# Kernel optimization log

Hardware: AMD Instinct MI355X
Metric: run time of the kernel (lower is better)

The kernel has to match this reference:

```python
import jax, jax.numpy as jnp
import numpy as np

EMBED_DIM = 1024
NUM_HEADS = 16
HEAD_DIM = EMBED_DIM // NUM_HEADS


def setup_inputs() -> dict:
    key = jax.random.key(0)
    ks = jax.random.split(key, 9)
    s = 1.0 / np.sqrt(EMBED_DIM)
    X = jax.random.normal(ks[0], (4, 2048, EMBED_DIM), dtype=jnp.float32)
    # Linear weights stored as [in, out] for x @ W + b
    Wq = jax.random.uniform(ks[1], (EMBED_DIM, EMBED_DIM), jnp.float32, -s, s)
    bq = jax.random.uniform(ks[2], (EMBED_DIM,), jnp.float32, -s, s)
    Wk = jax.random.uniform(ks[3], (EMBED_DIM, EMBED_DIM), jnp.float32, -s, s)
    bk = jax.random.uniform(ks[4], (EMBED_DIM,), jnp.float32, -s, s)
    Wv = jax.random.uniform(ks[5], (EMBED_DIM, EMBED_DIM), jnp.float32, -s, s)
    bv = jax.random.uniform(ks[6], (EMBED_DIM,), jnp.float32, -s, s)
    Wo = jax.random.uniform(ks[7], (EMBED_DIM, EMBED_DIM), jnp.float32, -s, s)
    bo = jax.random.uniform(ks[8], (EMBED_DIM,), jnp.float32, -s, s)
    return {"X": X, "Wq": Wq, "bq": bq, "Wk": Wk, "bk": bk,
            "Wv": Wv, "bv": bv, "Wo": Wo, "bo": bo}


def reference(X, Wq, bq, Wk, bk, Wv, bv, Wo, bo):
    B, S, _ = X.shape
    def split_heads(t):  # [B,S,E] -> [B,H,S,D]
        return t.reshape(B, S, NUM_HEADS, HEAD_DIM).transpose(0, 2, 1, 3)
    Q = split_heads(X @ Wq + bq)
    K = split_heads(X @ Wk + bk)
    V = split_heads(X @ Wv + bv)
    scale = 1.0 / np.sqrt(HEAD_DIM).astype(np.float32)
    scores = jnp.einsum('bhqd,bhkd->bhqk', Q, K) * scale
    probs = jax.nn.softmax(scores, axis=-1)
    attn = jnp.einsum('bhqk,bhkd->bhqd', probs, V)  # [B,H,S,D]
    combined = attn.transpose(0, 2, 1, 3).reshape(B, S, EMBED_DIM)
    return combined @ Wo + bo
```

## Files before the change

kernel.cpp:

```cpp
#include <hip/hip_runtime.h>
#include <hip/hip_bf16.h>

#define EMBED 1024
#define NHEADS 16
#define HDIM 64
#define SEQ 2048
#define BATCH 4
#define ROWS (BATCH * SEQ)

typedef __attribute__((ext_vector_type(8))) short bf16x8;
typedef __attribute__((ext_vector_type(4))) float f32x4;
typedef __attribute__((ext_vector_type(2))) float f32x2;
typedef __attribute__((ext_vector_type(16))) float f32x16;
typedef __attribute__((ext_vector_type(4))) unsigned int u32x4;
typedef __attribute__((ext_vector_type(2))) unsigned int u32x2;
typedef __attribute__((ext_vector_type(2))) int i32x2;
typedef unsigned int u32;

#define SL2E 0.18033688011112042f

__device__ __forceinline__ short f2bf(float f) {
    u32 u = __builtin_bit_cast(u32, f) + 0x8000u;
    return (short)(u >> 16);
}

__device__ __forceinline__ u32 pkbf(float a, float b) {
    u32 ua = __builtin_bit_cast(u32, a) + 0x8000u;
    u32 ub = __builtin_bit_cast(u32, b) + 0x8000u;
    return __builtin_amdgcn_perm(ua, ub, 0x03020706u);
}

__device__ __forceinline__ float fexp2(float x) {
#if __has_builtin(__builtin_amdgcn_exp2f)
    return __builtin_amdgcn_exp2f(x);
#else
    return exp2f(x);
#endif
}

__device__ __forceinline__ void async16(const void* g, void* l) {
    __builtin_amdgcn_global_load_lds((const __attribute__((address_space(1))) u32*)g,
                                     (__attribute__((address_space(3))) u32*)l, 16, 0, 0);
}

__global__ __launch_bounds__(256) void convert_f32_bf16(const float* __restrict__ in,
                                                        short* __restrict__ out) {
    int i = (blockIdx.x * 256 + threadIdx.x) * 4;
    float4 v = *(const float4*)&in[i];
    u32x2 o = { pkbf(v.x, v.y), pkbf(v.z, v.w) };
    *(u32x2*)&out[i] = o;
}

__global__ __launch_bounds__(256) void transpose_w4(const float* __restrict__ W0,
                                                    const float* __restrict__ W1,
                                                    const float* __restrict__ W2,
                                                    const float* __restrict__ W3,
                                                    short* __restrict__ T0,
                                                    short* __restrict__ T1,
                                                    short* __restrict__ T2,
                                                    short* __restrict__ T3) {
    const int z = blockIdx.z;
    const float* W = (z == 0) ? W0 : (z == 1) ? W1 : (z == 2) ? W2 : W3;
    short* WT = (z == 0) ? T0 : (z == 1) ? T1 : (z == 2) ? T2 : T3;
    const float sc = (z == 0) ? SL2E : 1.0f;
    __shared__ float T[64][65];
    const int k0 = blockIdx.y * 64, n0 = blockIdx.x * 64;
    const int rr = threadIdx.x >> 4, cc = (threadIdx.x & 15) * 4;
    #pragma unroll
    for (int p = 0; p < 4; ++p) {
        int r = p * 16 + rr;
        float4 v = *(const float4*)&W[(size_t)(k0 + r) * EMBED + n0 + cc];
        T[r][cc] = v.x * sc; T[r][cc + 1] = v.y * sc; T[r][cc + 2] = v.z * sc; T[r][cc + 3] = v.w * sc;
    }
    __syncthreads();
    #pragma unroll
    for (int p = 0; p < 4; ++p) {
        int r = p * 16 + rr;
        u32x2 o = { pkbf(T[cc][r], T[cc + 1][r]), pkbf(T[cc + 2][r], T[cc + 3][r]) };
        *(u32x2*)&WT[(size_t)(n0 + r) * EMBED + k0 + cc] = o;
    }
}

__global__ __launch_bounds__(512, 2) void gemm256(const short* __restrict__ A,
                                                  const short* __restrict__ BT,
                                                  const float* __restrict__ b0,
                                                  const float* __restrict__ b1,
                                                  const float* __restrict__ b2,
                                                  void* __restrict__ C0,
                                                  void* __restrict__ C1,
                                                  void* __restrict__ C2,
                                                  int mode) {
    __shared__ short As[2][16384];
    __shared__ short Bs[2][16384];
    const int tid = threadIdx.x;
    const int wid = tid >> 6, lane = tid & 63;
    const int c16 = lane & 15, quad = lane >> 4, sw = c16 & 7;
    const int wm = wid >> 2, wn = wid & 3;
    const int rowblk = blockIdx.y * 256, colblk = blockIdx.x * 256;

    const int r0 = tid >> 3;
    const int g0 = (tid & 7) ^ (r0 & 7);
    const short* aS0 = A + (size_t)(rowblk + r0) * EMBED + g0 * 8;
    const short* bS0 = BT + (size_t)(colblk + r0) * EMBED + g0 * 8;

#define STAGE_A(SBUF, H, V) do { \
    const short* _s = aS0 + (size_t)(H) * 131072 + (V) * 64; \
    async16(_s,         &As[SBUF][(H) * 8192 + wid * 512]); \
    async16(_s + 65536, &As[SBUF][(H) * 8192 + wid * 512 + 4096]); \
} while (0)
#define STAGE_B(SBUF, H, V) do { \
    const short* _s = bS0 + (size_t)(H) * 131072 + (V) * 64; \
    async16(_s,         &Bs[SBUF][(H) * 8192 + wid * 512]); \
    async16(_s + 65536, &Bs[SBUF][(H) * 8192 + wid * 512 + 4096]); \
} while (0)

    f32x4 acc[8][4] = {};
    bf16x8 aU[4][2], bE[2][2], bO[2][2];

#define LDA(BUF, MH) do { \
    _Pragma("unroll") \
    for (int fm = 0; fm < 4; ++fm) { \
        const int row = (MH) * 128 + wm * 64 + fm * 16 + c16; \
        _Pragma("unroll") \
        for (int ks = 0; ks < 2; ++ks) \
            aU[fm][ks] = *(const bf16x8*)&As[BUF][row * 64 + ((ks * 4 + quad) ^ sw) * 8]; \
    } \
} while (0)
#define LDB(BUF, NH, DST) do { \
    _Pragma("unroll") \
    for (int fn = 0; fn < 2; ++fn) { \
        const int rowb = (NH) * 128 + wn * 32 + fn * 16 + c16; \
        _Pragma("unroll") \
        for (int ks = 0; ks < 2; ++ks) \
            DST[fn][ks] = *(const bf16x8*)&Bs[BUF][rowb * 64 + ((ks * 4 + quad) ^ sw) * 8]; \
    } \
} while (0)
#define MM(MB, NB, BM_) do { \
    _Pragma("unroll") \
    for (int fm = 0; fm < 4; ++fm) \
        _Pragma("unroll") \
        for (int fn = 0; fn < 2; ++fn) \
            _Pragma("unroll") \
            for (int ks = 0; ks < 2; ++ks) \
                acc[(MB) + fm][(NB) + fn] = \
                    __builtin_amdgcn_mfma_f32_16x16x32_bf16(aU[fm][ks], BM_[fn][ks], \
                        acc[(MB) + fm][(NB) + fn], 0, 0, 0); \
} while (0)
#define PH_MID() do { \
    __builtin_amdgcn_s_barrier(); \
    asm volatile("s_waitcnt lgkmcnt(0)" ::: "memory"); \
    __builtin_amdgcn_s_setprio(1); \
} while (0)
#define PH_END(VM) do { \
    __builtin_amdgcn_s_setprio(0); \
    if (VM) asm volatile("s_waitcnt vmcnt(6)" ::: "memory"); \
    __builtin_amdgcn_s_barrier(); \
} while (0)

    STAGE_B(0, 0, 0); STAGE_A(0, 0, 0); STAGE_A(0, 1, 0); STAGE_B(0, 1, 0);
    STAGE_B(1, 0, 1); STAGE_A(1, 0, 1); STAGE_A(1, 1, 1);
    asm volatile("s_waitcnt vmcnt(6)" ::: "memory");
    __builtin_amdgcn_s_barrier();

    #pragma unroll 1
    for (int it = 0; it < 8; ++it) {
        const int u = 2 * it;
        const int v1 = u + 1, v2 = (u + 2) & 15, v3 = (u + 3) & 15;
        LDA(0, 0); LDB(0, 0, bE); STAGE_B(1, 1, v1); PH_MID(); MM(0, 0, bE); PH_END(0);
        LDB(0, 1, bO);            STAGE_B(0, 0, v2); PH_MID(); MM(0, 2, bO); PH_END(0);
        LDA(0, 1);                STAGE_A(0, 0, v2); PH_MID(); MM(4, 2, bO); PH_END(0);
                 STAGE_A(0, 1, v2); PH_MID(); MM(4, 0, bE); PH_END(1);
        LDA(1, 0); LDB(1, 0, bE); STAGE_B(0, 1, v2); PH_MID(); MM(0, 0, bE); PH_END(0);
        LDB(1, 1, bO);            STAGE_B(1, 0, v3); PH_MID(); MM(0, 2, bO); PH_END(0);
        LDA(1, 1);                STAGE_A(1, 0, v3); PH_MID(); MM(4, 2, bO); PH_END(0);
                 STAGE_A(1, 1, v3); PH_MID(); MM(4, 0, bE); PH_END(1);
    }

    asm volatile("s_waitcnt vmcnt(0)" ::: "memory");

    const int rb0 = rowblk + wm * 64 + quad * 4;
    const int cb0 = wn * 32 + c16;
    if (mode == 0) {
        const int z = colblk >> 10;
        const int cm = colblk & 1023;
        const float* bias = (z == 0) ? b0 : (z == 1) ? b1 : b2;
        if (z == 2) {
            short* Vt = (short*)C2;
            #pragma unroll
            for (int m = 0; m < 8; ++m) {
                const int row = rb0 + (m >> 2) * 128 + (m & 3) * 16;
                const int b = row >> 11, s = row & 2047;
                #pragma unroll
                for (int n = 0; n < 4; ++n) {
                    const int cv = cm + cb0 + (n >> 1) * 128 + (n & 1) * 16;
                    const int head = cv >> 6, d = cv & 63;
                    const float bv = bias[cv];
                    u32x2 o = { pkbf(acc[m][n][0] + bv, acc[m][n][1] + bv),
                                pkbf(acc[m][n][2] + bv, acc[m][n][3] + bv) };
                    *(u32x2*)&Vt[((size_t)(b * NHEADS + head) * HDIM + d) * SEQ + s] = o;
                }
            }
        } else {
            short* Cq = (short*)((z == 0) ? C0 : C1);
            const float bsc = (z == 0) ? SL2E : 1.0f;
            #pragma unroll
            for (int m = 0; m < 8; ++m) {
                const int row = rb0 + (m >> 2) * 128 + (m & 3) * 16;
                #pragma unroll
                for (int n = 0; n < 4; ++n) {
                    const int col = cm + cb0 + (n >> 1) * 128 + (n & 1) * 16;
                    const float bv = bias[col] * bsc;
                    #pragma unroll
                    for (int r = 0; r < 4; ++r)
                        Cq[(size_t)(row + r) * EMBED + col] = f2bf(acc[m][n][r] + bv);
                }
            }
        }
    } else {
        float* Co = (float*)C0;
        #pragma unroll
        for (int m = 0; m < 8; ++m) {
            const int row = rb0 + (m >> 2) * 128 + (m & 3) * 16;
            #pragma unroll
            for (int n = 0; n < 4; ++n) {
                const int col = colblk + cb0 + (n >> 1) * 128 + (n & 1) * 16;
                const float bv = b0[col];
                #pragma unroll
                for (int r = 0; r < 4; ++r)
                    Co[(size_t)(row + r) * EMBED + col] = acc[m][n][r] + bv;
            }
        }
    }
#undef PH_END
#undef PH_MID
#undef MM
#undef LDB
#undef LDA
#undef STAGE_A
#undef STAGE_B
}

__global__ __launch_bounds__(256, 5) void gemm_bf16_128(const short* __restrict__ A,
                                                        const short* __restrict__ BT0,
                                                        const short* __restrict__ BT1,
                                                        const short* __restrict__ BT2,
                                                        const float* __restrict__ b0,
                                                        const float* __restrict__ b1,
                                                        const float* __restrict__ b2,
                                                        void* __restrict__ C0,
                                                        void* __restrict__ C1,
                                                        void* __restrict__ C2,
                                                        int mode) {
    const int z = blockIdx.z;
    const short* BT = (z == 0) ? BT0 : (z == 1) ? BT1 : BT2;
    const float* bias = (z == 0) ? b0 : (z == 1) ? b1 : b2;
    const float bsc = (mode == 0 && z == 0) ? SL2E : 1.0f;
    __shared__ short As[128 * 64];
    __shared__ short Bs[64 * 64];
    const int tid = threadIdx.x;
    const int wave = tid >> 6, lane = tid & 63;
    const int c = lane & 15, quad = lane >> 4;
    const int sw = c & 7;
    const int row0 = blockIdx.y * 128, col0 = blockIdx.x * 64;
    f32x4 acc[2][4] = {};
    for (int k0 = 0; k0 < EMBED; k0 += 64) {
        #pragma unroll
        for (int it = 0; it < 4; ++it) {
            int ci = (it * 4 + wave) * 64 + lane;
            int row = ci >> 3, g = (ci & 7) ^ (row & 7);
            async16(&A[(size_t)(row0 + row) * EMBED + k0 + g * 8], &As[(it * 4 + wave) * 512]);
        }
        #pragma unroll
        for (int it = 0; it < 2; ++it) {
            int ci = (it * 4 + wave) * 64 + lane;
            int row = ci >> 3, g = (ci & 7) ^ (row & 7);
            async16(&BT[(size_t)(col0 + row) * EMBED + k0 + g * 8], &Bs[(it * 4 + wave) * 512]);
        }
        __syncthreads();
        #pragma unroll
        for (int ks = 0; ks < 2; ++ks) {
            bf16x8 af[2], bfr[4];
            #pragma unroll
            for (int i = 0; i < 2; ++i)
                af[i] = *(const bf16x8*)&As[(wave * 32 + i * 16 + c) * 64 + ((ks * 4 + quad) ^ sw) * 8];
            #pragma unroll
            for (int j = 0; j < 4; ++j)
                bfr[j] = *(const bf16x8*)&Bs[(j * 16 + c) * 64 + ((ks * 4 + quad) ^ sw) * 8];
            #pragma unroll
            for (int i = 0; i < 2; ++i)
                #pragma unroll
                for (int j = 0; j < 4; ++j)
                    acc[i][j] = __builtin_amdgcn_mfma_f32_16x16x32_bf16(af[i], bfr[j], acc[i][j], 0, 0, 0);
        }
        __syncthreads();
    }
    if (mode == 0 && z == 2) {
        short* Vt = (short*)C2;
        const int b = row0 >> 11, s0 = (row0 & 2047) + wave * 32;
        const int bh = b * NHEADS + blockIdx.x;
        #pragma unroll
        for (int i = 0; i < 2; ++i)
            #pragma unroll
            for (int j = 0; j < 4; ++j) {
                int d = j * 16 + c;
                float bv = bias[col0 + d];
                int s = s0 + i * 16 + quad * 4;
                u32x2 o = { pkbf(acc[i][j][0] + bv, acc[i][j][1] + bv),
                            pkbf(acc[i][j][2] + bv, acc[i][j][3] + bv) };
                *(u32x2*)&Vt[((size_t)bh * HDIM + d) * SEQ + s] = o;
            }
    } else {
        void* Cout = (z == 0) ? C0 : (z == 1) ? C1 : C2;
        #pragma unroll
        for (int i = 0; i < 2; ++i)
            #pragma unroll
            for (int j = 0; j < 4; ++j) {
                int colb = col0 + j * 16 + c;
                float bv = bias[colb] * bsc;
                #pragma unroll
                for (int r = 0; r < 4; ++r) {
                    int row = row0 + wave * 32 + i * 16 + quad * 4 + r;
                    float v = acc[i][j][r] + bv;
                    if (mode == 0) ((short*)Cout)[(size_t)row * EMBED + colb] = f2bf(v);
                    else           ((float*)Cout)[(size_t)row * EMBED + colb] = v;
                }
            }
    }
}

__global__ __launch_bounds__(256, 3) void attn_mfma(const short* __restrict__ Qb,
                                                    const short* __restrict__ Kb,
                                                    const short* __restrict__ Vt,
                                                    short* __restrict__ Ob) {
    __shared__ short SH[8192];
    short* Ks = SH;
    short* Vs = SH + 4096;
    const int tid = threadIdx.x;
    const int wave = tid >> 6, lane = tid & 63;
    const int l31 = lane & 31, h = lane >> 5;
    const int swz = l31 & 7;
    const int bh = blockIdx.y;
    const int b = bh >> 4, hd = bh & 15;
    const size_t base = (size_t)b * SEQ * EMBED + (size_t)hd * HDIM;
    const size_t vbase = (size_t)bh * HDIM * SEQ;
    const int q0 = blockIdx.x * 128;

    bf16x8 qf[4];
    #pragma unroll
    for (int ks = 0; ks < 4; ++ks)
        qf[ks] = *(const bf16x8*)&Qb[base + (size_t)(q0 + wave * 32 + l31) * EMBED + ks * 16 + h * 8];

    const short* kp[2];
    const short* vp[2];
    int ldofs[2];
    #pragma unroll
    for (int it = 0; it < 2; ++it) {
        int ci = (it * 4 + wave) * 64 + lane;
        int row = ci >> 3, g = (ci & 7) ^ (row & 7);
        kp[it] = Kb + base + (size_t)row * EMBED + g * 8;
        vp[it] = Vt + vbase + (size_t)row * SEQ + g * 8;
        ldofs[it] = (it * 4 + wave) * 512;
    }

    f32x16 O[2] = {};
    f32x2 ls = {0.0f, 0.0f};

    for (int kt = 0; kt < SEQ / 64; ++kt) {
        #pragma unroll
        for (int it = 0; it < 2; ++it) {
            async16(kp[it], &Ks[ldofs[it]]);
            async16(vp[it], &Vs[ldofs[it]]);
            kp[it] += 64 * EMBED;
            vp[it] += 64;
        }
        __syncthreads();

        f32x16 st[2] = {};
        #pragma unroll
        for (int nt = 0; nt < 2; ++nt)
            #pragma unroll
            for (int ks = 0; ks < 4; ++ks) {
                bf16x8 ak = *(const bf16x8*)&Ks[(nt * 32 + l31) * 64 + ((ks * 2 + h) ^ swz) * 8];
                st[nt] = __builtin_amdgcn_mfma_f32_32x32x16_bf16(ak, qf[ks], st[nt], 0, 0, 0);
            }

        u32 pk[2][8];
        #pragma unroll
        for (int nt = 0; nt < 2; ++nt)
            #pragma unroll
            for (int i = 0; i < 8; ++i) {
                float e0 = fexp2(st[nt][2 * i]), e1 = fexp2(st[nt][2 * i + 1]);
                f32x2 e = { e0, e1 };
                ls += e;
                pk[nt][i] = pkbf(e0, e1);
            }

        #pragma unroll
        for (int ks = 0; ks < 4; ++ks) {
            const int nt = ks >> 1, bs = (ks & 1) * 4;
            u32x4 fr;
#if __has_builtin(__builtin_amdgcn_permlane32_swap)
            i32x2 sA = __builtin_amdgcn_permlane32_swap((int)pk[nt][bs + 0], (int)pk[nt][bs + 2], false, false);
            i32x2 sB = __builtin_amdgcn_permlane32_swap((int)pk[nt][bs + 1], (int)pk[nt][bs + 3], false, false);
            fr.x = (u32)sA.x; fr.y = (u32)sB.x; fr.z = (u32)sA.y; fr.w = (u32)sB.y;
#else
            u32 s0 = h ? pk[nt][bs + 0] : pk[nt][bs + 2];
            u32 s1 = h ? pk[nt][bs + 1] : pk[nt][bs + 3];
            u32 r0 = (u32)__shfl_xor((int)s0, 32);
            u32 r1 = (u32)__shfl_xor((int)s1, 32);
            fr.x = h ? r0 : pk[nt][bs + 0];
            fr.y = h ? r1 : pk[nt][bs + 1];
            fr.z = h ? pk[nt][bs + 2] : r0;
            fr.w = h ? pk[nt][bs + 3] : r1;
#endif
            bf16x8 pf = __builtin_bit_cast(bf16x8, fr);
            #pragma unroll
            for (int mt = 0; mt < 2; ++mt) {
                bf16x8 vf = *(const bf16x8*)&Vs[(mt * 32 + l31) * 64 + ((ks * 2 + h) ^ swz) * 8];
                O[mt] = __builtin_amdgcn_mfma_f32_32x32x16_bf16(vf, pf, O[mt], 0, 0, 0);
            }
        }
        __syncthreads();
    }

    float lsum = ls.x + ls.y;
    lsum += __shfl_xor(lsum, 32);
    float inv = 1.0f / lsum;

    const int wbase = wave * 2048;
    #pragma unroll
    for (int mt = 0; mt < 2; ++mt)
        #pragma unroll
        for (int m = 0; m < 4; ++m) {
            u32x2 wv;
            wv.x = pkbf(O[mt][4 * m + 0] * inv, O[mt][4 * m + 1] * inv);
            wv.y = pkbf(O[mt][4 * m + 2] * inv, O[mt][4 * m + 3] * inv);
            int u = mt * 8 + 2 * m + h;
            int su = u ^ ((l31 & 7) << 1);
            *(u32x2*)&SH[wbase + l31 * 64 + su * 4] = wv;
        }
    __syncthreads();
    #pragma unroll
    for (int p = 0; p < 4; ++p) {
        int ci = p * 256 + tid;
        int wq = ci >> 8, rem = ci & 255;
        int r = rem >> 3, cch = rem & 7;
        int su = (2 * cch) ^ ((r & 7) << 1);
        bf16x8 val = *(const bf16x8*)&SH[wq * 2048 + r * 64 + su * 4];
        *(bf16x8*)&Ob[base + (size_t)(q0 + wq * 32 + r) * EMBED + cch * 8] = val;
    }
}

extern "C" void kernel_launch(void* const* d_in, const int* in_sizes, int n_in,
                              void* d_out, int out_size, void* d_ws, size_t ws_size,
                              hipStream_t stream)
{
    const float* X  = (const float*)d_in[0];
    const float* Wq = (const float*)d_in[1];
    const float* bq = (const float*)d_in[2];
    const float* Wk = (const float*)d_in[3];
    const float* bk = (const float*)d_in[4];
    const float* Wv = (const float*)d_in[5];
    const float* bv = (const float*)d_in[6];
    const float* Wo = (const float*)d_in[7];
    const float* bo = (const float*)d_in[8];
    float* out = (float*)d_out;

    const size_t NE = (size_t)ROWS * EMBED;
    short* Xbf = (short*)d_ws;
    short* Qb  = Xbf + NE;
    short* Kb  = Qb + NE;
    short* Vtb = Kb + NE;
    short* WqT = Vtb + NE;
    short* WkT = WqT + (size_t)EMBED * EMBED;
    short* WvT = WkT + (size_t)EMBED * EMBED;
    short* WoT = WvT + (size_t)EMBED * EMBED;

    convert_f32_bf16<<<(ROWS * EMBED) / 1024, 256, 0, stream>>>(X, Xbf);
    dim3 gw(16, 16, 4);
    transpose_w4<<<gw, 256, 0, stream>>>(Wq, Wk, Wv, Wo, WqT, WkT, WvT, WoT);

    dim3 gq(12, 32, 1);
    gemm256<<<gq, 512, 0, stream>>>(Xbf, WqT, bq, bk, bv, Qb, Kb, Vtb, 0);

    dim3 gt(SEQ / 128, BATCH * NHEADS);
    attn_mfma<<<gt, 256, 0, stream>>>(Qb, Kb, Vtb, Qb);

    dim3 gg(EMBED / 64, ROWS / 128, 1);
    gemm_bf16_128<<<gg, 256, 0, stream>>>(Qb, WoT, WoT, WoT, bo, bo, bo,
                                          out, out, out, 1);
}
```

Before: 276.8 us.

## Double-buffer attention K/V tiles, add MFMA priority, and swizzle block order

The attention kernel now double-buffers K/V tiles in shared memory, prefetching the next tile while computing the current one, with a single wait and barrier per iteration. It raises wave priority around the MFMA sections. The GEMM kernels and attention kernel also remap block indices so consecutive blocks are spread across XCD-sized groups to improve L2 locality. The double buffer doubles attention LDS use, which may reduce occupancy at 3 blocks per CU, and the hardcoded grid shapes in the remapping assume fixed launch dimensions.

```diff
diff --git a/kernel.cpp b/kernel.cpp
--- a/kernel.cpp
+++ b/kernel.cpp
@@ -96,7 +96,12 @@
     const int wid = tid >> 6, lane = tid & 63;
     const int c16 = lane & 15, quad = lane >> 4, sw = c16 & 7;
     const int wm = wid >> 2, wn = wid & 3;
-    const int rowblk = blockIdx.y * 256, colblk = blockIdx.x * 256;
+    const int gx = gridDim.x;
+    const int hid = blockIdx.y * gx + blockIdx.x;
+    const int cpx = (gx * gridDim.y) >> 3;
+    const int tle = (hid & 7) * cpx + (hid >> 3);
+    const int bx = tle % gx, by = tle / gx;
+    const int rowblk = by * 256, colblk = bx * 256;
 
     const int r0 = tid >> 3;
     const int g0 = (tid & 7) ^ (r0 & 7);
@@ -261,7 +266,10 @@
     const int wave = tid >> 6, lane = tid & 63;
     const int c = lane & 15, quad = lane >> 4;
     const int sw = c & 7;
-    const int row0 = blockIdx.y * 128, col0 = blockIdx.x * 64;
+    const int hid = blockIdx.y * 16 + blockIdx.x;
+    const int tle = (hid & 7) * 128 + (hid >> 3);
+    const int bx = tle & 15, by = tle >> 4;
+    const int row0 = by * 128, col0 = bx * 64;
     f32x4 acc[2][4] = {};
     for (int k0 = 0; k0 < EMBED; k0 += 64) {
         #pragma unroll
@@ -297,7 +305,7 @@
     if (mode == 0 && z == 2) {
         short* Vt = (short*)C2;
         const int b = row0 >> 11, s0 = (row0 & 2047) + wave * 32;
-        const int bh = b * NHEADS + blockIdx.x;
+        const int bh = b * NHEADS + bx;
         #pragma unroll
         for (int i = 0; i < 2; ++i)
             #pragma unroll
@@ -332,18 +340,18 @@
                                                     const short* __restrict__ Kb,
                                                     const short* __restrict__ Vt,
                                                     short* __restrict__ Ob) {
-    __shared__ short SH[8192];
-    short* Ks = SH;
-    short* Vs = SH + 4096;
+    __shared__ short SH[16384];
     const int tid = threadIdx.x;
     const int wave = tid >> 6, lane = tid & 63;
     const int l31 = lane & 31, h = lane >> 5;
     const int swz = l31 & 7;
-    const int bh = blockIdx.y;
+    const int hid = blockIdx.y * 16 + blockIdx.x;
+    const int tle = (hid & 7) * 128 + (hid >> 3);
+    const int qb = tle & 15, bh = tle >> 4;
     const int b = bh >> 4, hd = bh & 15;
     const size_t base = (size_t)b * SEQ * EMBED + (size_t)hd * HDIM;
     const size_t vbase = (size_t)bh * HDIM * SEQ;
-    const int q0 = blockIdx.x * 128;
+    const int q0 = qb * 128;
 
     bf16x8 qf[4];
     #pragma unroll
@@ -365,17 +373,34 @@
     f32x16 O[2] = {};
     f32x2 ls = {0.0f, 0.0f};
 
+    #pragma unroll
+    for (int it = 0; it < 2; ++it) {
+        async16(kp[it], &SH[ldofs[it]]);
+        async16(vp[it], &SH[8192 + ldofs[it]]);
+        kp[it] += 64 * EMBED;
+        vp[it] += 64;
+    }
+    asm volatile("s_waitcnt vmcnt(0)" ::: "memory");
+    __builtin_amdgcn_s_barrier();
+
+    #pragma unroll 2
     for (int kt = 0; kt < SEQ / 64; ++kt) {
-        #pragma unroll
-        for (int it = 0; it < 2; ++it) {
-            async16(kp[it], &Ks[ldofs[it]]);
-            async16(vp[it], &Vs[ldofs[it]]);
-            kp[it] += 64 * EMBED;
-            vp[it] += 64;
-        }
-        __syncthreads();
+        const int bo = (kt & 1) * 4096;
+        const short* Ks = SH + bo;
+        const short* Vs = SH + 8192 + bo;
+        if (kt < SEQ / 64 - 1) {
+            const int nbo = 4096 - bo;
+            #pragma unroll
+            for (int it = 0; it < 2; ++it) {
+                async16(kp[it], &SH[nbo + ldofs[it]]);
+                async16(vp[it], &SH[8192 + nbo + ldofs[it]]);
+                kp[it] += 64 * EMBED;
+                vp[it] += 64;
+            }
+        }
 
         f32x16 st[2] = {};
+        __builtin_amdgcn_s_setprio(1);
         #pragma unroll
         for (int nt = 0; nt < 2; ++nt)
             #pragma unroll
@@ -383,6 +408,7 @@
                 bf16x8 ak = *(const bf16x8*)&Ks[(nt * 32 + l31) * 64 + ((ks * 2 + h) ^ swz) * 8];
                 st[nt] = __builtin_amdgcn_mfma_f32_32x32x16_bf16(ak, qf[ks], st[nt], 0, 0, 0);
             }
+        __builtin_amdgcn_s_setprio(0);
 
         u32 pk[2][8];
         #pragma unroll
@@ -395,6 +421,7 @@
                 pk[nt][i] = pkbf(e0, e1);
             }
 
+        __builtin_amdgcn_s_setprio(1);
         #pragma unroll
         for (int ks = 0; ks < 4; ++ks) {
             const int nt = ks >> 1, bs = (ks & 1) * 4;
@@ -420,7 +447,10 @@
                 O[mt] = __builtin_amdgcn_mfma_f32_32x32x16_bf16(vf, pf, O[mt], 0, 0, 0);
             }
         }
-        __syncthreads();
+        __builtin_amdgcn_s_setprio(0);
+
+        asm volatile("s_waitcnt vmcnt(0)" ::: "memory");
+        __builtin_amdgcn_s_barrier();
     }
 
     float lsum = ls.x + ls.y;
```

Result: no change. 278.7 us (+0.7%).
